# Performance work log

Hardware: AMD Instinct MI355X
Metric: run time of the kernel (lower is better)

The kernel has to match this reference:

```python
import jax, jax.numpy as jnp
import numpy as np

B, T, D, H = 4, 4096, 1024, 16
CAP = 0.5


def setup_inputs() -> dict:
    key = jax.random.key(0)
    ks = jax.random.split(key, 8)
    s = 0.02
    n = lambda k, shape: jax.random.normal(k, shape, dtype=jnp.float32) * s
    return {
        "x": jax.random.normal(ks[0], (B, T, D), dtype=jnp.float32),
        "w_router": n(ks[1], (D,)),
        "in_proj_w": n(ks[2], (3 * D, D)),
        "in_proj_b": jnp.zeros((3 * D,), jnp.float32),
        "out_proj_w": n(ks[3], (D, D)),
        "out_proj_b": jnp.zeros((D,), jnp.float32),
        "w1": n(ks[4], (4 * D, D)),
        "b1": jnp.zeros((4 * D,), jnp.float32),
        "w2": n(ks[5], (D, 4 * D)),
        "b2": jnp.zeros((D,), jnp.float32),
        "ln1_g": jnp.ones((D,), jnp.float32),
        "ln1_b": jnp.zeros((D,), jnp.float32),
        "ln2_g": jnp.ones((D,), jnp.float32),
        "ln2_b": jnp.zeros((D,), jnp.float32),
    }


def _ln(x, g, b, eps=1e-5):
    mu = jnp.mean(x, -1, keepdims=True)
    var = jnp.var(x, -1, keepdims=True)  # population variance, matches torch LayerNorm
    return (x - mu) * jax.lax.rsqrt(var + eps) * g + b


def reference(x, w_router, in_proj_w, in_proj_b, out_proj_w, out_proj_b,
              w1, b1, w2, b2, ln1_g, ln1_b, ln2_g, ln2_b):
    Bx, Tx, Dx = x.shape
    k = max(1, int(Tx * CAP))  # tokens routed through the block, same k for every batch row
    logits = x @ w_router  # (B,T) scalar router scores
    aux = jnp.mean(logits ** 2) * 0.01
    # top-k selection; sort indices ascending = boolean-mask gather order in torch
    idx = jnp.sort(jax.lax.top_k(logits, k)[1], axis=-1)  # (B,k)
    xs = jnp.take_along_axis(x, idx[:, :, None], axis=1)  # (B,k,D)

    h = _ln(xs, ln1_g, ln1_b)
    qkv = h @ in_proj_w.T + in_proj_b  # (B,k,3D)
    q, kk, v = jnp.split(qkv, 3, axis=-1)
    dh = Dx // H
    heads = lambda t: t.reshape(Bx, k, H, dh).transpose(0, 2, 1, 3)  # (B,H,k,dh)
    q, kk, v = heads(q), heads(kk), heads(v)
    scores = jnp.einsum('bhqd,bhkd->bhqk', q, kk) / jnp.sqrt(jnp.float32(dh))
    attn = jax.nn.softmax(scores, axis=-1)
    o = jnp.einsum('bhqk,bhkd->bhqd', attn, v).transpose(0, 2, 1, 3).reshape(Bx, k, Dx)
    o = o @ out_proj_w.T + out_proj_b
    xs = xs + o
    h2 = _ln(xs, ln2_g, ln2_b)
    ff = jax.nn.gelu(h2 @ w1.T + b1, approximate=False) @ w2.T + b2
    xs = xs + ff
    # scatter processed tokens back; unselected tokens pass through unchanged
    out = x.at[jnp.arange(Bx)[:, None], idx].set(xs)
    return out, aux
```

## Files before the change

kernel.cpp:

```cpp
#include <hip/hip_runtime.h>

#define B_    4
#define T_    4096
#define D_    1024
#define H_    16
#define DH_   64
#define KTOK  2048
#define MROWS (B_*KTOK)

typedef unsigned short u16;
typedef __attribute__((ext_vector_type(8))) short short8;
typedef __attribute__((ext_vector_type(4))) float f32x4;
typedef __attribute__((ext_vector_type(4))) unsigned int u32x4;
typedef __attribute__((ext_vector_type(2))) unsigned int u32x2;
typedef __attribute__((ext_vector_type(4))) unsigned short u16x4;

static __device__ __forceinline__ u16 f2bf(float f) {
  union { float f; unsigned int u; } a; a.f = f;
  unsigned int u = a.u;
  unsigned int r = (u + 0x7FFFu + ((u >> 16) & 1u)) >> 16;
  return (u16)r;
}

#if defined(__has_builtin)
#if __has_builtin(__builtin_amdgcn_exp2f)
#define EXP2F(x) __builtin_amdgcn_exp2f(x)
#endif
#endif
#ifndef EXP2F
#define EXP2F(x) exp2f(x)
#endif

static __device__ __forceinline__ unsigned int pkbf_t(float a, float b) {
  unsigned int ua = __builtin_bit_cast(unsigned int, a);
  unsigned int ub = __builtin_bit_cast(unsigned int, b);
  return __builtin_amdgcn_perm(ub, ua, 0x07060302u);
}

static __device__ __forceinline__ void gld_lds16(const u16* g, u16* l) {
  __builtin_amdgcn_global_load_lds((__attribute__((address_space(1))) void*)g,
                                   (__attribute__((address_space(3))) void*)l, 16, 0, 0);
}

__global__ void __launch_bounds__(256) router_kernel(const float* __restrict__ x,
    const float* __restrict__ wr, float* __restrict__ logits, float* __restrict__ auxacc)
{
  int tid = threadIdx.x; int lane = tid & 63, wave = tid >> 6;
  int row = blockIdx.x * 4 + wave;
  const float* xr = x + (size_t)row * D_;
  float dot = 0.f;
#pragma unroll
  for (int j = 0; j < 4; j++) {
    int c = j * 256 + lane * 4;
    f32x4 xv = *(const f32x4*)(xr + c);
    f32x4 wv = *(const f32x4*)(wr + c);
    dot += xv[0]*wv[0] + xv[1]*wv[1] + xv[2]*wv[2] + xv[3]*wv[3];
  }
#pragma unroll
  for (int d = 1; d < 64; d <<= 1) dot += __shfl_xor(dot, d);
  __shared__ float red[4];
  if (lane == 0) { logits[row] = dot; red[wave] = dot; }
  __syncthreads();
  if (tid == 0) {
    float a = red[0]*red[0] + red[1]*red[1] + red[2]*red[2] + red[3]*red[3];
    atomicAdd(auxacc, a);
  }
}

__global__ void __launch_bounds__(256) rank_kernel(const float* __restrict__ logits,
    int* __restrict__ mask, int* __restrict__ idx,
    const float* __restrict__ acc, float* __restrict__ auxout)
{
  __shared__ float ll[T_];
  int b = blockIdx.y;
  int tid = threadIdx.x;
  if (b == 0 && blockIdx.x == 0 && tid == 0)
    auxout[0] = acc[0] * (0.01f / (float)(B_ * T_));
  const float* lg = logits + (size_t)b * T_;
  for (int j = tid; j < T_; j += 256) ll[j] = lg[j];
  __syncthreads();
  int t = blockIdx.x * 256 + tid;
  float my = ll[t];
  int rank = 0;
  for (int j = 0; j < T_; j += 4) {
    f32x4 lj = *(const f32x4*)&ll[j];
    rank += (lj[0] > my) || (lj[0] == my && (j+0) < t);
    rank += (lj[1] > my) || (lj[1] == my && (j+1) < t);
    rank += (lj[2] > my) || (lj[2] == my && (j+2) < t);
    rank += (lj[3] > my) || (lj[3] == my && (j+3) < t);
  }
  int sel = (rank < KTOK) ? 1 : 0;
  mask[(size_t)b * T_ + t] = sel;
  if (sel) idx[b * KTOK + rank] = t;
}

__global__ void __launch_bounds__(256) passthru_kernel(const float* __restrict__ x,
    const int* __restrict__ mask, float* __restrict__ out)
{
  int row = blockIdx.x;
  if (mask[row]) return;
  const float* s = x + (size_t)row * D_;
  float* d = out + (size_t)row * D_;
  *(f32x4*)(d + threadIdx.x * 4) = *(const f32x4*)(s + threadIdx.x * 4);
}

template<bool GATHER>
__global__ void __launch_bounds__(256) ln_kernel(const float* __restrict__ src,
    const int* __restrict__ idx, const float* __restrict__ g, const float* __restrict__ bb,
    float* __restrict__ xs_out, u16* __restrict__ hout)
{
  int row = blockIdx.x;
  int tid = threadIdx.x;
  const float* srow;
  if (GATHER) {
    int b = row >> 11, i = row & (KTOK - 1);
    int t = idx[b * KTOK + i];
    srow = src + ((size_t)b * T_ + t) * D_;
  } else {
    srow = src + (size_t)row * D_;
  }
  f32x4 v = *(const f32x4*)(srow + tid * 4);
  float s  = v[0] + v[1] + v[2] + v[3];
  float sq = v[0]*v[0] + v[1]*v[1] + v[2]*v[2] + v[3]*v[3];
#pragma unroll
  for (int d = 1; d < 64; d <<= 1) { s += __shfl_xor(s, d); sq += __shfl_xor(sq, d); }
  __shared__ float rs[4], rq[4];
  int lane = tid & 63, wave = tid >> 6;
  if (lane == 0) { rs[wave] = s; rq[wave] = sq; }
  __syncthreads();
  s  = rs[0] + rs[1] + rs[2] + rs[3];
  sq = rq[0] + rq[1] + rq[2] + rq[3];
  float mean = s * (1.0f / D_);
  float var  = sq * (1.0f / D_) - mean * mean;
  float rstd = rsqrtf(var + 1e-5f);
  f32x4 gg = *(const f32x4*)(g + tid * 4);
  f32x4 bv = *(const f32x4*)(bb + tid * 4);
  if (GATHER) *(f32x4*)(xs_out + (size_t)row * D_ + tid * 4) = v;
  u16x4 o;
#pragma unroll
  for (int j = 0; j < 4; j++) o[j] = f2bf((v[j] - mean) * rstd * gg[j] + bv[j]);
  *(u16x4*)(hout + (size_t)row * D_ + tid * 4) = o;
}

__global__ void __launch_bounds__(256) f2bf_all(const float* __restrict__ s0, const float* __restrict__ s1,
    const float* __restrict__ s2, const float* __restrict__ s3,
    u16* __restrict__ d0, u16* __restrict__ d1, u16* __restrict__ d2, u16* __restrict__ d3)
{
  const size_t c0 = (size_t)3 * D_ * D_, c1 = (size_t)4 * D_ * D_, c2 = (size_t)8 * D_ * D_;
  size_t e = (size_t)blockIdx.x * 1024 + (size_t)threadIdx.x * 4;
  const float* s; u16* d; size_t off;
  if (e < c0)      { s = s0; d = d0; off = e; }
  else if (e < c1) { s = s1; d = d1; off = e - c0; }
  else if (e < c2) { s = s2; d = d2; off = e - c1; }
  else             { s = s3; d = d3; off = e - c2; }
  f32x4 v = *(const f32x4*)(s + off);
  u16x4 o; o[0]=f2bf(v[0]); o[1]=f2bf(v[1]); o[2]=f2bf(v[2]); o[3]=f2bf(v[3]);
  *(u16x4*)(d + off) = o;
}

template<int EPI>
__global__ void __launch_bounds__(256, 2) gemm_bt(
    const u16* __restrict__ A, const u16* __restrict__ W,
    const float* __restrict__ bias, float* __restrict__ xs,
    u16* __restrict__ Cb, float* __restrict__ outf,
    const int* __restrict__ idx, u16* __restrict__ vtb, int M, int N, int K)
{
  __shared__ u16 As[128 * 32];
  __shared__ u16 Ws[128 * 32];
  const int tid = threadIdx.x;
  const int lane = tid & 63, wave = tid >> 6;
  const int wm = wave >> 1, wn = wave & 1;
  const int m16 = lane & 15, quad = lane >> 4;

  const size_t arow0 = (size_t)blockIdx.y * 128;
  const size_t wrow0 = (size_t)blockIdx.x * 128;
  const int r4 = lane >> 2, c8 = (lane & 3) * 8;

  const u16* ag0 = A + (arow0 + wave * 16 + r4) * (size_t)K + c8;
  const u16* ag1 = ag0 + (size_t)64 * K;
  const u16* wg0 = W + (wrow0 + wave * 16 + r4) * (size_t)K + c8;
  const u16* wg1 = wg0 + (size_t)64 * K;
  u16* la0 = As + (wave * 16) * 32;
  u16* la1 = As + (64 + wave * 16) * 32;
  u16* lw0 = Ws + (wave * 16) * 32;
  u16* lw1 = Ws + (64 + wave * 16) * 32;

  f32x4 acc[4][4];
#pragma unroll
  for (int i = 0; i < 4; i++)
#pragma unroll
    for (int j = 0; j < 4; j++) acc[i][j] = (f32x4)0.0f;

  for (int k0 = 0; k0 < K; k0 += 32) {
    gld_lds16(ag0 + k0, la0);
    gld_lds16(ag1 + k0, la1);
    gld_lds16(wg0 + k0, lw0);
    gld_lds16(wg1 + k0, lw1);
    __syncthreads();
    short8 af[4], wf[4];
#pragma unroll
    for (int mt = 0; mt < 4; mt++)
      af[mt] = *(const short8*)(As + (wm * 64 + mt * 16 + m16) * 32 + quad * 8);
#pragma unroll
    for (int nt = 0; nt < 4; nt++)
      wf[nt] = *(const short8*)(Ws + (wn * 64 + nt * 16 + m16) * 32 + quad * 8);
#pragma unroll
    for (int mt = 0; mt < 4; mt++)
#pragma unroll
      for (int nt = 0; nt < 4; nt++)
        acc[mt][nt] = __builtin_amdgcn_mfma_f32_16x16x32_bf16(af[mt], wf[nt], acc[mt][nt], 0, 0, 0);
    __syncthreads();
  }

#pragma unroll
  for (int mt = 0; mt < 4; mt++) {
#pragma unroll
    for (int nt = 0; nt < 4; nt++) {
      f32x4 a = acc[mt][nt];
      size_t col = wrow0 + wn * 64 + nt * 16 + m16;
      float bvv = bias[col];
      size_t rowb = arow0 + wm * 64 + mt * 16 + quad * 4;
      if (EPI == 0) {
        if ((int)col < 2 * D_) {
          float sc = ((int)col < D_) ? 0.18033688f : 1.0f;
#pragma unroll
          for (int r = 0; r < 4; r++)
            Cb[(rowb + r) * (size_t)N + col] = f2bf((a[r] + bvv) * sc);
        } else {
          int hdh = (int)col - 2 * D_;
          int bb  = (int)(rowb >> 11);
          int tok = (int)(rowb & (KTOK - 1));
          u16x4 o;
#pragma unroll
          for (int r = 0; r < 4; r++) o[r] = f2bf(a[r] + bvv);
          *(u16x4*)&vtb[(((size_t)(bb * H_) + (hdh >> 6)) * 64 + (hdh & 63)) * KTOK + tok] = o;
        }
      } else if (EPI == 1) {
#pragma unroll
        for (int r = 0; r < 4; r++) {
          size_t o = (rowb + r) * (size_t)N + col;
          xs[o] = xs[o] + (a[r] + bvv);
        }
      } else if (EPI == 2) {
#pragma unroll
        for (int r = 0; r < 4; r++) {
          float v = a[r] + bvv;
          float gv = 0.5f * v * (1.0f + erff(v * 0.70710678118654752f));
          Cb[(rowb + r) * (size_t)N + col] = f2bf(gv);
        }
      } else {
#pragma unroll
        for (int r = 0; r < 4; r++) {
          size_t row = rowb + r;
          int b = (int)(row >> 11);
          int i = (int)(row & (KTOK - 1));
          int t = idx[b * KTOK + i];
          float vv = xs[row * (size_t)D_ + col] + (a[r] + bvv);
          outf[((size_t)b * T_ + t) * D_ + col] = vv;
        }
      }
    }
  }
}

#define PSTR 72
__global__ void __launch_bounds__(256, 3) attn_kernel(const u16* __restrict__ qkv,
                                                      const u16* __restrict__ vtb,
                                                      u16* __restrict__ obuf)
{
  __shared__ u16 Ks[2][64 * 64];
  __shared__ u16 Vs[2][64 * 64];
  __shared__ u16 Ps[4][16 * PSTR];

  const int tid = threadIdx.x;
  const int lane = tid & 63, wave = tid >> 6;
  const int m16 = lane & 15, quad = lane >> 4;
  const int bh = blockIdx.x;
  const int b = bh >> 4, h = bh & 15;
  const int q0 = blockIdx.y * 128 + wave * 32;

  const u16* base = qkv + ((size_t)b * KTOK) * (3 * D_) + h * DH_;
  const u16* vb   = vtb + (size_t)bh * 64 * KTOK;

  short8 qf[2][2];
#pragma unroll
  for (int qh = 0; qh < 2; qh++) {
    const u16* qrow = base + (size_t)(q0 + qh * 16 + m16) * (3 * D_);
    qf[qh][0] = *(const short8*)(qrow + quad * 8);
    qf[qh][1] = *(const short8*)(qrow + 32 + quad * 8);
  }

  f32x4 oacc[2][4];
#pragma unroll
  for (int qh = 0; qh < 2; qh++)
#pragma unroll
    for (int nt = 0; nt < 4; nt++) oacc[qh][nt] = (f32x4)0.0f;
  f32x4 lsum[2] = {(f32x4)0.0f, (f32x4)0.0f};

  auto stage_tile = [&](const u16* g0, size_t rstride, u16* lds) {
#pragma unroll
    for (int c = 0; c < 2; c++) {
      int g = c * 256 + tid;
      int key = g >> 3;
      int cc = (g ^ key) & 7;
      gld_lds16(g0 + (size_t)key * rstride + cc * 8,
                lds + (size_t)(c * 256 + (tid & ~63)) * 8);
    }
  };

  stage_tile(base + D_, 3 * D_, &Ks[0][0]);
  stage_tile(vb, KTOK, &Vs[0][0]);
  __syncthreads();

  int buf = 0;
  for (int tk = 0; tk < KTOK; tk += 64) {
    if (tk + 64 < KTOK) {
      stage_tile(base + (size_t)(tk + 64) * (3 * D_) + D_, 3 * D_, &Ks[buf ^ 1][0]);
      stage_tile(vb + (tk + 64), KTOK, &Vs[buf ^ 1][0]);
    }
    const u16* Kb = &Ks[buf][0];
    const u16* Vb = &Vs[buf][0];

    f32x4 sacc[2][4];
#pragma unroll
    for (int qh = 0; qh < 2; qh++)
#pragma unroll
      for (int nt = 0; nt < 4; nt++) sacc[qh][nt] = (f32x4)0.0f;
    __builtin_amdgcn_s_setprio(1);
#pragma unroll
    for (int nt = 0; nt < 4; nt++) {
      int row = nt * 16 + m16;
      int sw = row & 7;
      short8 kf0 = *(const short8*)&Kb[row * 64 + ((quad ^ sw) * 8)];
      short8 kf1 = *(const short8*)&Kb[row * 64 + (((4 + quad) ^ sw) * 8)];
#pragma unroll
      for (int qh = 0; qh < 2; qh++) {
        sacc[qh][nt] = __builtin_amdgcn_mfma_f32_16x16x32_bf16(kf0, qf[qh][0], sacc[qh][nt], 0, 0, 0);
        sacc[qh][nt] = __builtin_amdgcn_mfma_f32_16x16x32_bf16(kf1, qf[qh][1], sacc[qh][nt], 0, 0, 0);
      }
    }
    __builtin_amdgcn_s_setprio(0);

    short8 vf[4][2];
#pragma unroll
    for (int nt = 0; nt < 4; nt++) {
      int row = nt * 16 + m16;
      int sw = row & 7;
      vf[nt][0] = *(const short8*)&Vb[row * 64 + ((quad ^ sw) * 8)];
      vf[nt][1] = *(const short8*)&Vb[row * 64 + (((4 + quad) ^ sw) * 8)];
    }

#pragma unroll
    for (int qh = 0; qh < 2; qh++) {
#pragma unroll
      for (int nt = 0; nt < 4; nt++) {
        f32x4 p;
#pragma unroll
        for (int r = 0; r < 4; r++) p[r] = EXP2F(sacc[qh][nt][r]);
        lsum[qh] += p;
        u32x2 w2; w2[0] = pkbf_t(p[0], p[1]); w2[1] = pkbf_t(p[2], p[3]);
        *(u32x2*)&Ps[wave][m16 * PSTR + nt * 16 + quad * 4] = w2;
      }
      short8 pa0 = *(const short8*)&Ps[wave][m16 * PSTR + quad * 8];
      short8 pa1 = *(const short8*)&Ps[wave][m16 * PSTR + 32 + quad * 8];
      __builtin_amdgcn_s_setprio(1);
#pragma unroll
      for (int nt = 0; nt < 4; nt++) {
        oacc[qh][nt] = __builtin_amdgcn_mfma_f32_16x16x32_bf16(pa0, vf[nt][0], oacc[qh][nt], 0, 0, 0);
        oacc[qh][nt] = __builtin_amdgcn_mfma_f32_16x16x32_bf16(pa1, vf[nt][1], oacc[qh][nt], 0, 0, 0);
      }
      __builtin_amdgcn_s_setprio(0);
    }

    __syncthreads();
    buf ^= 1;
  }

  float rl[2][4];
#pragma unroll
  for (int qh = 0; qh < 2; qh++) {
    float l = (lsum[qh][0] + lsum[qh][1]) + (lsum[qh][2] + lsum[qh][3]);
    l += __shfl_xor(l, 16);
    l += __shfl_xor(l, 32);
#pragma unroll
    for (int r = 0; r < 4; r++) {
      float lr = __shfl(l, (lane & 48) | (quad * 4 + r));
      rl[qh][r] = 1.0f / lr;
    }
  }

#pragma unroll
  for (int qh = 0; qh < 2; qh++)
#pragma unroll
    for (int nt = 0; nt < 4; nt++)
#pragma unroll
      for (int r = 0; r < 4; r++) {
        int qq = q0 + qh * 16 + quad * 4 + r;
        float v = oacc[qh][nt][r] * rl[qh][r];
        obuf[((size_t)b * KTOK + qq) * D_ + h * DH_ + nt * 16 + m16] = f2bf(v);
      }
}

extern "C" void kernel_launch(void* const* d_in, const int* in_sizes, int n_in,
                              void* d_out, int out_size, void* d_ws, size_t ws_size,
                              hipStream_t stream)
{
  (void)in_sizes; (void)n_in; (void)out_size; (void)ws_size;
  const float* x          = (const float*)d_in[0];
  const float* w_router   = (const float*)d_in[1];
  const float* in_proj_w  = (const float*)d_in[2];
  const float* in_proj_b  = (const float*)d_in[3];
  const float* out_proj_w = (const float*)d_in[4];
  const float* out_proj_b = (const float*)d_in[5];
  const float* w1         = (const float*)d_in[6];
  const float* b1         = (const float*)d_in[7];
  const float* w2         = (const float*)d_in[8];
  const float* b2         = (const float*)d_in[9];
  const float* ln1g       = (const float*)d_in[10];
  const float* ln1b       = (const float*)d_in[11];
  const float* ln2g       = (const float*)d_in[12];
  const float* ln2b       = (const float*)d_in[13];
  float* out = (float*)d_out;

  char* w = (char*)d_ws;
  auto alloc = [&](size_t bytes) -> char* {
    char* p = w; w += (bytes + 255) & ~(size_t)255; return p;
  };
  float* logits = (float*)alloc((size_t)B_ * T_ * 4);
  int*   mask   = (int*)  alloc((size_t)B_ * T_ * 4);
  int*   idx    = (int*)  alloc((size_t)B_ * KTOK * 4);
  float* auxacc = (float*)alloc(256);
  u16* inpw  = (u16*)alloc((size_t)3 * D_ * D_ * 2);
  u16* outpw = (u16*)alloc((size_t)D_ * D_ * 2);
  u16* w1b   = (u16*)alloc((size_t)4 * D_ * D_ * 2);
  u16* w2b   = (u16*)alloc((size_t)4 * D_ * D_ * 2);
  float* xs  = (float*)alloc((size_t)MROWS * D_ * 4);
  u16* hbuf  = (u16*)alloc((size_t)MROWS * D_ * 2);
  char* region = alloc((size_t)MROWS * 4 * D_ * 2);
  u16* qkvb = (u16*)region;
  u16* obuf = (u16*)(region + (size_t)MROWS * 3 * D_ * 2);
  u16* ffb  = (u16*)region;
  u16* vtb  = (u16*)alloc((size_t)B_ * H_ * DH_ * KTOK * 2);

  (void)hipMemsetAsync(auxacc, 0, 4, stream);

  router_kernel<<<B_ * T_ / 4, 256, 0, stream>>>(x, w_router, logits, auxacc);
  rank_kernel<<<dim3(T_ / 256, B_), 256, 0, stream>>>(logits, mask, idx, auxacc,
                                                      out + (size_t)B_ * T_ * D_);
  passthru_kernel<<<B_ * T_, 256, 0, stream>>>(x, mask, out);
  ln_kernel<true><<<MROWS, 256, 0, stream>>>(x, idx, ln1g, ln1b, xs, hbuf);

  f2bf_all<<<12 * D_ * D_ / 1024, 256, 0, stream>>>(in_proj_w, out_proj_w, w1, w2,
                                                    inpw, outpw, w1b, w2b);

  gemm_bt<0><<<dim3(3 * D_ / 128, MROWS / 128), 256, 0, stream>>>(
      hbuf, inpw, in_proj_b, nullptr, qkvb, nullptr, nullptr, vtb, MROWS, 3 * D_, D_);
  attn_kernel<<<dim3(B_ * H_, KTOK / 128), 256, 0, stream>>>(qkvb, vtb, obuf);
  gemm_bt<1><<<dim3(D_ / 128, MROWS / 128), 256, 0, stream>>>(
      obuf, outpw, out_proj_b, xs, nullptr, nullptr, nullptr, nullptr, MROWS, D_, D_);
  ln_kernel<false><<<MROWS, 256, 0, stream>>>(xs, nullptr, ln2g, ln2b, nullptr, hbuf);
  gemm_bt<2><<<dim3(4 * D_ / 128, MROWS / 128), 256, 0, stream>>>(
      hbuf, w1b, b1, nullptr, ffb, nullptr, nullptr, nullptr, MROWS, 4 * D_, D_);
  gemm_bt<3><<<dim3(D_ / 128, MROWS / 128), 256, 0, stream>>>(
      ffb, w2b, b2, xs, nullptr, out, idx, nullptr, MROWS, D_, 4 * D_);
}
```

Baseline: 749.8 us.

## Double-buffer GEMM LDS tiles and remap block IDs across XCDs

The GEMM kernel now keeps two LDS buffers for the A and W tiles and issues the next k-slice's global-to-LDS loads before computing on the current slice. This is meant to hide global-memory latency behind the MFMA work. Block IDs are also remapped so consecutive tiles are grouped per XCD (id&7 interleave), which is meant to improve L2 reuse. LDS use doubles to 32KB per block, which may hurt occupancy at 2 blocks per CU. The remap assumes the grid size is divisible by 8.

```diff
diff --git a/kernel.cpp b/kernel.cpp
--- a/kernel.cpp
+++ b/kernel.cpp
@@ -165,25 +165,34 @@
     u16* __restrict__ Cb, float* __restrict__ outf,
     const int* __restrict__ idx, u16* __restrict__ vtb, int M, int N, int K)
 {
-  __shared__ u16 As[128 * 32];
-  __shared__ u16 Ws[128 * 32];
+  __shared__ u16 As[2][128 * 32];
+  __shared__ u16 Ws[2][128 * 32];
   const int tid = threadIdx.x;
   const int lane = tid & 63, wave = tid >> 6;
   const int wm = wave >> 1, wn = wave & 1;
   const int m16 = lane & 15, quad = lane >> 4;
 
-  const size_t arow0 = (size_t)blockIdx.y * 128;
-  const size_t wrow0 = (size_t)blockIdx.x * 128;
+  const int gx = gridDim.x;
+  const int id = blockIdx.y * gx + blockIdx.x;
+  const int cpx = (gx * (int)gridDim.y) >> 3;
+  const int tl = (id & 7) * cpx + (id >> 3);
+  const int bx = tl % gx, by = tl / gx;
+
+  const size_t arow0 = (size_t)by * 128;
+  const size_t wrow0 = (size_t)bx * 128;
   const int r4 = lane >> 2, c8 = (lane & 3) * 8;
 
   const u16* ag0 = A + (arow0 + wave * 16 + r4) * (size_t)K + c8;
   const u16* ag1 = ag0 + (size_t)64 * K;
   const u16* wg0 = W + (wrow0 + wave * 16 + r4) * (size_t)K + c8;
   const u16* wg1 = wg0 + (size_t)64 * K;
-  u16* la0 = As + (wave * 16) * 32;
-  u16* la1 = As + (64 + wave * 16) * 32;
-  u16* lw0 = Ws + (wave * 16) * 32;
-  u16* lw1 = Ws + (64 + wave * 16) * 32;
+
+  auto stage = [&](int k0, int s) {
+    gld_lds16(ag0 + k0, &As[s][0] + (wave * 16) * 32);
+    gld_lds16(ag1 + k0, &As[s][0] + (64 + wave * 16) * 32);
+    gld_lds16(wg0 + k0, &Ws[s][0] + (wave * 16) * 32);
+    gld_lds16(wg1 + k0, &Ws[s][0] + (64 + wave * 16) * 32);
+  };
 
   f32x4 acc[4][4];
 #pragma unroll
@@ -191,25 +200,25 @@
 #pragma unroll
     for (int j = 0; j < 4; j++) acc[i][j] = (f32x4)0.0f;
 
+  stage(0, 0);
+  __syncthreads();
+  int cur = 0;
   for (int k0 = 0; k0 < K; k0 += 32) {
-    gld_lds16(ag0 + k0, la0);
-    gld_lds16(ag1 + k0, la1);
-    gld_lds16(wg0 + k0, lw0);
-    gld_lds16(wg1 + k0, lw1);
-    __syncthreads();
+    if (k0 + 32 < K) stage(k0 + 32, cur ^ 1);
     short8 af[4], wf[4];
 #pragma unroll
     for (int mt = 0; mt < 4; mt++)
-      af[mt] = *(const short8*)(As + (wm * 64 + mt * 16 + m16) * 32 + quad * 8);
+      af[mt] = *(const short8*)(&As[cur][0] + (wm * 64 + mt * 16 + m16) * 32 + quad * 8);
 #pragma unroll
     for (int nt = 0; nt < 4; nt++)
-      wf[nt] = *(const short8*)(Ws + (wn * 64 + nt * 16 + m16) * 32 + quad * 8);
+      wf[nt] = *(const short8*)(&Ws[cur][0] + (wn * 64 + nt * 16 + m16) * 32 + quad * 8);
 #pragma unroll
     for (int mt = 0; mt < 4; mt++)
 #pragma unroll
       for (int nt = 0; nt < 4; nt++)
         acc[mt][nt] = __builtin_amdgcn_mfma_f32_16x16x32_bf16(af[mt], wf[nt], acc[mt][nt], 0, 0, 0);
     __syncthreads();
+    cur ^= 1;
   }
 
 #pragma unroll
```

Result: no change. 747.2 us (-0.3%).
